# Kernel tuning notes

Measured on AMD Instinct MI355X. Metric: run time of the kernel, lower is better.

The kernel has to match this reference:

```python
import jax, jax.numpy as jnp
import numpy as np

N, E, F_IN, H, G, C, L = 100000, 1600000, 128, 128, 1000, 10, 3
EPS = 1e-5


def setup_inputs() -> dict:
    key = jax.random.key(0)
    ks = jax.random.split(key, 10)
    x = jax.random.normal(ks[0], (N, F_IN), dtype=jnp.float32)
    edge_index = jax.random.randint(ks[1], (2, E), 0, N, dtype=jnp.int64)
    batch = jnp.sort(jax.random.randint(ks[2], (N,), 0, G, dtype=jnp.int64))
    s = 1.0 / np.sqrt(H)
    conv_w = jax.random.normal(ks[3], (L, F_IN, H), dtype=jnp.float32) * s
    conv_b = jnp.zeros((L, H), dtype=jnp.float32)
    bn_gamma = jnp.ones((L, H), dtype=jnp.float32)
    bn_beta = jnp.zeros((L, H), dtype=jnp.float32)
    w1 = jax.random.normal(ks[4], (H, H // 2), dtype=jnp.float32) * s
    b1 = jnp.zeros((H // 2,), dtype=jnp.float32)
    w2 = jax.random.normal(ks[5], (H // 2, C), dtype=jnp.float32) * (1.0 / np.sqrt(H // 2))
    b2 = jnp.zeros((C,), dtype=jnp.float32)
    return {"x": x, "conv_w": conv_w, "conv_b": conv_b, "bn_gamma": bn_gamma,
            "bn_beta": bn_beta, "w1": w1, "b1": b1, "w2": w2, "b2": b2,
            "edge_index": edge_index, "batch": batch}


def _gcn_conv(x, w, b, src, dst):
    # PyG GCNConv: h = x @ W; symmetric-normalized aggregation with self-loops.
    h = x @ w  # [N, H]
    deg = 1.0 + jax.ops.segment_sum(jnp.ones((E,), x.dtype), dst, num_segments=N)
    dinv = jax.lax.rsqrt(deg)  # [N]
    norm = dinv[src] * dinv[dst]  # [E]
    agg = jax.ops.segment_sum(h[src] * norm[:, None], dst, num_segments=N)
    agg = agg + h * (dinv * dinv)[:, None]  # self-loop contribution
    return agg + b


def _batchnorm(x, gamma, beta):
    mean = jnp.mean(x, axis=0)
    var = jnp.mean(jnp.square(x - mean), axis=0)  # biased, as in torch BN fwd
    return gamma * (x - mean) * jax.lax.rsqrt(var + EPS) + beta


def reference(x, conv_w, conv_b, bn_gamma, bn_beta, w1, b1, w2, b2, edge_index, batch):
    src, dst = edge_index[0], edge_index[1]
    h = x
    for i in range(L):
        h = _gcn_conv(h, conv_w[i], conv_b[i], src, dst)
        h = _batchnorm(h, bn_gamma[i], bn_beta[i])
        h = jax.nn.relu(h)  # dropout is identity in eval mode
    # global mean pool over graphs
    sums = jax.ops.segment_sum(h, batch, num_segments=G)
    cnts = jax.ops.segment_sum(jnp.ones((N,), h.dtype), batch, num_segments=G)
    pooled = sums / jnp.maximum(cnts, 1.0)[:, None]
    # classifier MLP
    z = jax.nn.relu(pooled @ w1 + b1)
    return z @ w2 + b2
```

## Files before the change

kernel.cpp:

```cpp
#include <hip/hip_runtime.h>
#include <hip/hip_bf16.h>

#define N_NODES 100000
#define N_EDGES 1600000
#define HDIM    128
#define NGRAPH  1000
#define NCLASS  10
#define BN_EPS  1e-5f

#define BSHIFT  7
#define BMASK   127
#define NBUCKET 782
#define TILE3   8192
#define NSB     196
#define GATHER_BLOCKS 1024

typedef short short8_t __attribute__((ext_vector_type(8)));
typedef float f32x4_t  __attribute__((ext_vector_type(4)));

__device__ __forceinline__ float bf2f(ushort u) {
    union { unsigned int i; float f; } v; v.i = ((unsigned int)u) << 16; return v.f;
}
__device__ __forceinline__ ushort f2bf(float f) {
    union { float f; unsigned int i; } v; v.f = f;
    unsigned int i = v.i;
    unsigned int r = i + 0x7fffu + ((i >> 16) & 1u);
    return (ushort)(r >> 16);
}
__device__ __forceinline__ unsigned int pack2(float a, float b) {
    return (unsigned int)f2bf(a) | ((unsigned int)f2bf(b) << 16);
}
__device__ __forceinline__ float lo16(unsigned int u) {
    union { unsigned int i; float f; } v; v.i = u << 16; return v.f;
}
__device__ __forceinline__ float hi16(unsigned int u) {
    union { unsigned int i; float f; } v; v.i = u & 0xffff0000u; return v.f;
}

__global__ __launch_bounds__(256)
void wprep_hist(const float* __restrict__ W, ushort* __restrict__ wtbT,
                const int* __restrict__ dst, int* __restrict__ blockhist) {
    __shared__ int h[NBUCKET];
    int t = threadIdx.x;
    if (blockIdx.x < 48) {
        int l = blockIdx.x >> 4, slice = blockIdx.x & 15;
        int idx = slice * 1024 + t * 4;
        int k = idx >> 7, n = idx & 127;
        float4 w4 = *(const float4*)&W[(size_t)l * 16384 + k * 128 + n];
        ushort* o = wtbT + (size_t)l * 16384;
        o[(n + 0) * 128 + k] = f2bf(w4.x);
        o[(n + 1) * 128 + k] = f2bf(w4.y);
        o[(n + 2) * 128 + k] = f2bf(w4.z);
        o[(n + 3) * 128 + k] = f2bf(w4.w);
        return;
    }
    int blk = blockIdx.x - 48;
    for (int i = t; i < NBUCKET; i += 256) h[i] = 0;
    __syncthreads();
    long tile0 = (long)blk * TILE3;
    #pragma unroll 4
    for (int i = 0; i < TILE3 / 256; i++) {
        long e = tile0 + t + i * 256;
        if (e < N_EDGES) atomicAdd(&h[dst[e] >> BSHIFT], 1);
    }
    __syncthreads();
    for (int b = t; b < NBUCKET; b += 256)
        blockhist[(size_t)b * NSB + blk] = h[b];
}

__global__ __launch_bounds__(64)
void col_scan(int* __restrict__ blockhist, int* __restrict__ coltotal) {
    int b = blockIdx.x;
    int lane = threadIdx.x;
    int base = b * NSB;
    int carry = 0;
    for (int r = 0; r < NSB; r += 64) {
        int i = r + lane;
        int v = (i < NSB) ? blockhist[base + i] : 0;
        int x = v;
        #pragma unroll
        for (int off = 1; off < 64; off <<= 1) {
            int y = __shfl_up(x, off, 64);
            if (lane >= off) x += y;
        }
        if (i < NSB) blockhist[base + i] = carry + x - v;
        carry += __shfl(x, 63, 64);
    }
    if (lane == 0) coltotal[b] = carry;
}

__global__ __launch_bounds__(1024)
void bucket_scan(const int* __restrict__ coltotal, int* __restrict__ bucket_base,
                 int* __restrict__ row_start) {
    __shared__ int wsum[16];
    int t = threadIdx.x, lane = t & 63, wid = t >> 6;
    int v = (t < NBUCKET) ? coltotal[t] : 0;
    int x = v;
    #pragma unroll
    for (int off = 1; off < 64; off <<= 1) {
        int y = __shfl_up(x, off, 64);
        if (lane >= off) x += y;
    }
    if (lane == 63) wsum[wid] = x;
    __syncthreads();
    if (t == 0) {
        int s = 0;
        #pragma unroll
        for (int w = 0; w < 16; w++) { int tmp = wsum[w]; wsum[w] = s; s += tmp; }
    }
    __syncthreads();
    int excl = wsum[wid] + (x - v);
    if (t < NBUCKET) bucket_base[t] = excl;
    if (t == 0) { bucket_base[NBUCKET] = N_EDGES; row_start[N_NODES] = N_EDGES; }
}

__global__ __launch_bounds__(256)
void scatter_pairs(const int* __restrict__ src, const int* __restrict__ dst,
                   const int* __restrict__ bucket_base, const int* __restrict__ blockhist,
                   unsigned int* __restrict__ pairs) {
    __shared__ int lbase[NBUCKET];
    __shared__ int lcur[NBUCKET];
    int t = threadIdx.x;
    int blk = blockIdx.x;
    for (int b = t; b < NBUCKET; b += 256) {
        lbase[b] = bucket_base[b] + blockhist[(size_t)b * NSB + blk];
        lcur[b] = 0;
    }
    __syncthreads();
    long tile0 = (long)blk * TILE3;
    #pragma unroll 4
    for (int i = 0; i < TILE3 / 256; i++) {
        long e = tile0 + t + i * 256;
        if (e < N_EDGES) {
            int d = dst[e];
            int bkt = d >> BSHIFT;
            int p = atomicAdd(&lcur[bkt], 1);
            pairs[lbase[bkt] + p] = (unsigned int)src[e] | ((unsigned int)(d & BMASK) << 24);
        }
    }
}

__global__ __launch_bounds__(256)
void build_csr(const unsigned int* __restrict__ pairs, const int* __restrict__ bucket_base,
               int* __restrict__ row_start, int* __restrict__ csr_src, float* __restrict__ dinv) {
    __shared__ int hist[128];
    __shared__ int cur[128];
    __shared__ int wsum[2];
    int b = blockIdx.x;
    int t = threadIdx.x;
    int beg = bucket_base[b], end = bucket_base[b + 1];
    if (t < 128) hist[t] = 0;
    __syncthreads();
    for (int e = beg + t; e < end; e += 256)
        atomicAdd(&hist[pairs[e] >> 24], 1);
    __syncthreads();
    int v = 0, x = 0;
    int lane = t & 63, wid = t >> 6;
    if (t < 128) {
        v = hist[t];
        x = v;
        #pragma unroll
        for (int off = 1; off < 64; off <<= 1) {
            int y = __shfl_up(x, off, 64);
            if (lane >= off) x += y;
        }
        if (lane == 63) wsum[wid] = x;
    }
    __syncthreads();
    if (t == 0) { int s = wsum[0]; wsum[0] = 0; wsum[1] = s; }
    __syncthreads();
    if (t < 128) {
        int excl = wsum[wid] + (x - v);
        cur[t] = excl;
        int node = b * 128 + t;
        if (node < N_NODES) {
            row_start[node] = beg + excl;
            dinv[node] = rsqrtf(1.0f + (float)v);
        }
    }
    __syncthreads();
    for (int e = beg + t; e < end; e += 256) {
        unsigned int pk = pairs[e];
        int ln = pk >> 24;
        int sp = atomicAdd(&cur[ln], 1);
        csr_src[beg + sp] = (int)(pk & 0xFFFFFFu);
    }
}

__global__ __launch_bounds__(256)
void gemm_mfma(const float* __restrict__ inf, const ushort* __restrict__ inb,
               const ushort* __restrict__ wtbT, const float* __restrict__ bnp,
               const float* __restrict__ dinv, ushort* __restrict__ out) {
    __shared__ ushort as_[64][136];
    __shared__ ushort wt[128][136];
    int t = threadIdx.x;
    int wave = t >> 6, lane = t & 63;
    int g = lane >> 4, c = lane & 15;
    int rowbase = blockIdx.x * 64;

    #pragma unroll
    for (int i = 0; i < 8; i++) {
        int cid = t + i * 256;
        int n = cid >> 4, ko = (cid & 15) * 8;
        uint4 v = *(const uint4*)&wtbT[n * 128 + ko];
        *(uint4*)&wt[n][ko] = v;
    }
    if (inf) {
        #pragma unroll
        for (int i = 0; i < 8; i++) {
            int cid = t + i * 256;
            int r = cid >> 5, co = (cid & 31) * 4;
            int row = rowbase + r;
            ushort4 pk = make_ushort4(0, 0, 0, 0);
            if (row < N_NODES) {
                float4 v = *(const float4*)&inf[(size_t)row * HDIM + co];
                pk.x = f2bf(v.x); pk.y = f2bf(v.y); pk.z = f2bf(v.z); pk.w = f2bf(v.w);
            }
            *(ushort4*)&as_[r][co] = pk;
        }
    } else {
        #pragma unroll
        for (int i = 0; i < 4; i++) {
            int cid = t + i * 256;
            int r = cid >> 4, co = (cid & 15) * 8;
            int row = rowbase + r;
            uint4 o = make_uint4(0, 0, 0, 0);
            if (row < N_NODES) {
                uint4 p = *(const uint4*)&inb[(size_t)row * HDIM + co];
                float4 scA = *(const float4*)&bnp[co];
                float4 scB = *(const float4*)&bnp[co + 4];
                float4 shA = *(const float4*)&bnp[128 + co];
                float4 shB = *(const float4*)&bnp[132 + co];
                float v0 = fmaxf(0.f, fmaf(lo16(p.x), scA.x, shA.x));
                float v1 = fmaxf(0.f, fmaf(hi16(p.x), scA.y, shA.y));
                float v2 = fmaxf(0.f, fmaf(lo16(p.y), scA.z, shA.z));
                float v3 = fmaxf(0.f, fmaf(hi16(p.y), scA.w, shA.w));
                float v4 = fmaxf(0.f, fmaf(lo16(p.z), scB.x, shB.x));
                float v5 = fmaxf(0.f, fmaf(hi16(p.z), scB.y, shB.y));
                float v6 = fmaxf(0.f, fmaf(lo16(p.w), scB.z, shB.z));
                float v7 = fmaxf(0.f, fmaf(hi16(p.w), scB.w, shB.w));
                o.x = pack2(v0, v1); o.y = pack2(v2, v3);
                o.z = pack2(v4, v5); o.w = pack2(v6, v7);
            }
            *(uint4*)&as_[r][co] = o;
        }
    }
    __syncthreads();

    int m0 = wave * 16;
    short8_t a[4];
    #pragma unroll
    for (int ch = 0; ch < 4; ch++)
        a[ch] = *(const short8_t*)&as_[m0 + c][ch * 32 + g * 8];
    f32x4_t acc[8] = {};
    #pragma unroll
    for (int ct = 0; ct < 8; ct++) {
        #pragma unroll
        for (int ch = 0; ch < 4; ch++) {
            short8_t b = *(const short8_t*)&wt[ct * 16 + c][ch * 32 + g * 8];
            acc[ct] = __builtin_amdgcn_mfma_f32_16x16x32_bf16(a[ch], b, acc[ct], 0, 0, 0);
        }
    }
    float dv[4];
    #pragma unroll
    for (int reg = 0; reg < 4; reg++) {
        int rr = rowbase + m0 + g * 4 + reg;
        dv[reg] = dinv[rr < N_NODES ? rr : 0];
    }
    __syncthreads();
    #pragma unroll
    for (int ct = 0; ct < 8; ct++)
        #pragma unroll
        for (int reg = 0; reg < 4; reg++)
            as_[m0 + g * 4 + reg][ct * 16 + c] = f2bf(acc[ct][reg] * dv[reg]);
    __syncthreads();
    #pragma unroll
    for (int i = 0; i < 8; i++) {
        int cid = t + i * 256;
        int r = cid >> 5, co = (cid & 31) * 4;
        int row = rowbase + r;
        if (row < N_NODES)
            *(ushort4*)&out[(size_t)row * HDIM + co] = *(const ushort4*)&as_[r][co];
    }
}

__global__ __launch_bounds__(256)
void gather_agg(const ushort* __restrict__ hw, const int* __restrict__ row_start,
                const int* __restrict__ csr_src, const float* __restrict__ dinv,
                const float* __restrict__ bias, ushort* __restrict__ aggout,
                float* __restrict__ Spart, float* __restrict__ Qpart) {
    __shared__ float s_sum[128];
    __shared__ float s_sq[128];
    int t = threadIdx.x;
    if (t < 128) { s_sum[t] = 0.f; s_sq[t] = 0.f; }
    __syncthreads();
    int lane = t & 63, wid = t >> 6;
    int g = lane >> 4, c = lane & 15;
    int fo = c * 8;
    float4 bA = *(const float4*)&bias[fo];
    float4 bB = *(const float4*)&bias[fo + 4];
    float ls[8] = {}, lq[8] = {};
    int gw = blockIdx.x * 4 + wid;
    int nw = gridDim.x * 4;
    for (int n = gw; n < N_NODES; n += nw) {
        int jb = row_start[n], je = row_start[n + 1];
        float acc[8] = {};
        int j = jb;
        for (; j + 16 <= je; j += 16) {
            int s0 = csr_src[j + 4 * g + 0];
            int s1 = csr_src[j + 4 * g + 1];
            int s2 = csr_src[j + 4 * g + 2];
            int s3 = csr_src[j + 4 * g + 3];
            uint4 p0 = *(const uint4*)&hw[(size_t)s0 * HDIM + fo];
            uint4 p1 = *(const uint4*)&hw[(size_t)s1 * HDIM + fo];
            uint4 p2 = *(const uint4*)&hw[(size_t)s2 * HDIM + fo];
            uint4 p3 = *(const uint4*)&hw[(size_t)s3 * HDIM + fo];
            acc[0] += (lo16(p0.x) + lo16(p1.x)) + (lo16(p2.x) + lo16(p3.x));
            acc[1] += (hi16(p0.x) + hi16(p1.x)) + (hi16(p2.x) + hi16(p3.x));
            acc[2] += (lo16(p0.y) + lo16(p1.y)) + (lo16(p2.y) + lo16(p3.y));
            acc[3] += (hi16(p0.y) + hi16(p1.y)) + (hi16(p2.y) + hi16(p3.y));
            acc[4] += (lo16(p0.z) + lo16(p1.z)) + (lo16(p2.z) + lo16(p3.z));
            acc[5] += (hi16(p0.z) + hi16(p1.z)) + (hi16(p2.z) + hi16(p3.z));
            acc[6] += (lo16(p0.w) + lo16(p1.w)) + (lo16(p2.w) + lo16(p3.w));
            acc[7] += (hi16(p0.w) + hi16(p1.w)) + (hi16(p2.w) + hi16(p3.w));
        }
        for (; j + 8 <= je; j += 8) {
            int sa = csr_src[j + 2 * g];
            int sb = csr_src[j + 2 * g + 1];
            uint4 p = *(const uint4*)&hw[(size_t)sa * HDIM + fo];
            uint4 q = *(const uint4*)&hw[(size_t)sb * HDIM + fo];
            acc[0] += lo16(p.x) + lo16(q.x);
            acc[1] += hi16(p.x) + hi16(q.x);
            acc[2] += lo16(p.y) + lo16(q.y);
            acc[3] += hi16(p.y) + hi16(q.y);
            acc[4] += lo16(p.z) + lo16(q.z);
            acc[5] += hi16(p.z) + hi16(q.z);
            acc[6] += lo16(p.w) + lo16(q.w);
            acc[7] += hi16(p.w) + hi16(q.w);
        }
        int e0 = j + g, e1 = j + 4 + g;
        if (e0 < je) {
            int s = csr_src[e0];
            uint4 p = *(const uint4*)&hw[(size_t)s * HDIM + fo];
            acc[0] += lo16(p.x); acc[1] += hi16(p.x);
            acc[2] += lo16(p.y); acc[3] += hi16(p.y);
            acc[4] += lo16(p.z); acc[5] += hi16(p.z);
            acc[6] += lo16(p.w); acc[7] += hi16(p.w);
        }
        if (e1 < je) {
            int s = csr_src[e1];
            uint4 p = *(const uint4*)&hw[(size_t)s * HDIM + fo];
            acc[0] += lo16(p.x); acc[1] += hi16(p.x);
            acc[2] += lo16(p.y); acc[3] += hi16(p.y);
            acc[4] += lo16(p.z); acc[5] += hi16(p.z);
            acc[6] += lo16(p.w); acc[7] += hi16(p.w);
        }
        #pragma unroll
        for (int i = 0; i < 8; i++) {
            acc[i] += __shfl_xor(acc[i], 16);
            acc[i] += __shfl_xor(acc[i], 32);
        }
        uint4 ps = *(const uint4*)&hw[(size_t)n * HDIM + fo];
        float dn = dinv[n];
        float r[8];
        r[0] = fmaf(acc[0] + lo16(ps.x), dn, bA.x);
        r[1] = fmaf(acc[1] + hi16(ps.x), dn, bA.y);
        r[2] = fmaf(acc[2] + lo16(ps.y), dn, bA.z);
        r[3] = fmaf(acc[3] + hi16(ps.y), dn, bA.w);
        r[4] = fmaf(acc[4] + lo16(ps.z), dn, bB.x);
        r[5] = fmaf(acc[5] + hi16(ps.z), dn, bB.y);
        r[6] = fmaf(acc[6] + lo16(ps.w), dn, bB.z);
        r[7] = fmaf(acc[7] + hi16(ps.w), dn, bB.w);
        if (g == 0) {
            uint4 o;
            o.x = pack2(r[0], r[1]); o.y = pack2(r[2], r[3]);
            o.z = pack2(r[4], r[5]); o.w = pack2(r[6], r[7]);
            *(uint4*)&aggout[(size_t)n * HDIM + fo] = o;
            #pragma unroll
            for (int i = 0; i < 8; i++) { ls[i] += r[i]; lq[i] += r[i] * r[i]; }
        }
    }
    if (g == 0) {
        #pragma unroll
        for (int i = 0; i < 8; i++) {
            atomicAdd(&s_sum[fo + i], ls[i]);
            atomicAdd(&s_sq[fo + i],  lq[i]);
        }
    }
    __syncthreads();
    if (t < 128) {
        Spart[(size_t)blockIdx.x * 128 + t] = s_sum[t];
        Qpart[(size_t)blockIdx.x * 128 + t] = s_sq[t];
    }
}

__global__ __launch_bounds__(256)
void bn_reduce_prep(const float* __restrict__ Spart, const float* __restrict__ Qpart,
                    const float* __restrict__ gamma, const float* __restrict__ beta,
                    float* __restrict__ bnp) {
    __shared__ float rs[32][8];
    __shared__ float rq[32][8];
    int t = threadIdx.x;
    int fi = t & 7, chunk = t >> 3;
    int f = blockIdx.x * 8 + fi;
    float s = 0.f, q = 0.f;
    for (int b = chunk; b < GATHER_BLOCKS; b += 32) {
        s += Spart[(size_t)b * 128 + f];
        q += Qpart[(size_t)b * 128 + f];
    }
    rs[chunk][fi] = s; rq[chunk][fi] = q;
    __syncthreads();
    if (t < 8) {
        float S = 0.f, Q = 0.f;
        #pragma unroll
        for (int cc = 0; cc < 32; cc++) { S += rs[cc][t]; Q += rq[cc][t]; }
        int ff = blockIdx.x * 8 + t;
        float mean = S * (1.0f / N_NODES);
        float var  = Q * (1.0f / N_NODES) - mean * mean;
        float inv  = rsqrtf(var + BN_EPS);
        float sc   = gamma[ff] * inv;
        bnp[ff]       = sc;
        bnp[128 + ff] = beta[ff] - mean * sc;
    }
}

__global__ __launch_bounds__(128)
void pool_mlp(const ushort* __restrict__ agg, const float* __restrict__ bnp,
              const int* __restrict__ batch, const float* __restrict__ w1,
              const float* __restrict__ b1, const float* __restrict__ w2,
              const float* __restrict__ b2, float* __restrict__ out) {
    __shared__ float p[128];
    __shared__ float z[64];
    int g = blockIdx.x;
    int k = threadIdx.x;
    int lo = 0, hi = N_NODES;
    while (lo < hi) { int mid = (lo + hi) >> 1; if (batch[mid] < g) lo = mid + 1; else hi = mid; }
    int start = lo;
    hi = N_NODES;
    while (lo < hi) { int mid = (lo + hi) >> 1; if (batch[mid] < g + 1) lo = mid + 1; else hi = mid; }
    int end = lo;
    float sc = bnp[k], sh = bnp[128 + k];
    float sum = 0.f;
    int n = start;
    for (; n + 4 <= end; n += 4) {
        float a0 = bf2f(agg[(size_t)(n + 0) * HDIM + k]);
        float a1 = bf2f(agg[(size_t)(n + 1) * HDIM + k]);
        float a2 = bf2f(agg[(size_t)(n + 2) * HDIM + k]);
        float a3 = bf2f(agg[(size_t)(n + 3) * HDIM + k]);
        sum += fmaxf(0.f, fmaf(a0, sc, sh));
        sum += fmaxf(0.f, fmaf(a1, sc, sh));
        sum += fmaxf(0.f, fmaf(a2, sc, sh));
        sum += fmaxf(0.f, fmaf(a3, sc, sh));
    }
    for (; n < end; n++)
        sum += fmaxf(0.f, fmaf(bf2f(agg[(size_t)n * HDIM + k]), sc, sh));
    float cnt = (float)(end - start);
    p[k] = sum / fmaxf(cnt, 1.0f);
    __syncthreads();
    if (k < 64) {
        float s = b1[k];
        #pragma unroll 8
        for (int kk = 0; kk < 128; kk++) s += p[kk] * w1[kk * 64 + k];
        z[k] = fmaxf(0.f, s);
    }
    __syncthreads();
    if (k < NCLASS) {
        float s = b2[k];
        #pragma unroll
        for (int j = 0; j < 64; j++) s += z[j] * w2[j * NCLASS + k];
        out[g * NCLASS + k] = s;
    }
}

extern "C" void kernel_launch(void* const* d_in, const int* in_sizes, int n_in,
                              void* d_out, int out_size, void* d_ws, size_t ws_size,
                              hipStream_t stream) {
    const float* x      = (const float*)d_in[0];
    const float* conv_w = (const float*)d_in[1];
    const float* conv_b = (const float*)d_in[2];
    const float* gamma  = (const float*)d_in[3];
    const float* beta   = (const float*)d_in[4];
    const float* w1     = (const float*)d_in[5];
    const float* b1     = (const float*)d_in[6];
    const float* w2     = (const float*)d_in[7];
    const float* b2     = (const float*)d_in[8];
    const int*   ei     = (const int*)d_in[9];
    const int*   batch  = (const int*)d_in[10];
    float* out = (float*)d_out;

    char* ws = (char*)d_ws;
    size_t off = 0;
    auto alloc = [&](size_t bytes) -> void* {
        off = (off + 255) & ~(size_t)255;
        void* p = ws + off;
        off += bytes;
        return p;
    };
    ushort* A         = (ushort*)alloc((size_t)N_NODES * HDIM * 2);
    ushort* aggB      = (ushort*)alloc((size_t)N_NODES * HDIM * 2);
    int*    csr_src   = (int*)   alloc((size_t)N_EDGES * 4);
    int*    row_start = (int*)   alloc((size_t)(N_NODES + 1) * 4);
    float*  dinv      = (float*) alloc((size_t)N_NODES * 4);
    int*    blockhist = (int*)   alloc((size_t)NBUCKET * NSB * 4);
    int*    coltotal  = (int*)   alloc((size_t)NBUCKET * 4);
    int*    bbase     = (int*)   alloc((size_t)(NBUCKET + 1) * 4);
    ushort* wtbT      = (ushort*)alloc((size_t)3 * 16384 * 2);
    float*  Spart     = (float*) alloc((size_t)GATHER_BLOCKS * 128 * 4);
    float*  Qpart     = (float*) alloc((size_t)GATHER_BLOCKS * 128 * 4);
    float*  bnp       = (float*) alloc(3 * 256 * 4);
    unsigned int* pairs = (unsigned int*)aggB;

    const int* srcv = ei;
    const int* dstv = ei + N_EDGES;

    wprep_hist   <<<48 + NSB, 256, 0, stream>>>(conv_w, wtbT, dstv, blockhist);
    col_scan     <<<NBUCKET, 64, 0, stream>>>(blockhist, coltotal);
    bucket_scan  <<<1, 1024, 0, stream>>>(coltotal, bbase, row_start);
    scatter_pairs<<<NSB, 256, 0, stream>>>(srcv, dstv, bbase, blockhist, pairs);
    build_csr    <<<NBUCKET, 256, 0, stream>>>(pairs, bbase, row_start, csr_src, dinv);

    for (int l = 0; l < 3; l++) {
        gemm_mfma<<<(N_NODES + 63) / 64, 256, 0, stream>>>(
            (l == 0) ? x : nullptr, (l == 0) ? nullptr : aggB,
            wtbT + (size_t)l * 16384,
            (l == 0) ? nullptr : (bnp + (l - 1) * 256), dinv, A);
        gather_agg<<<GATHER_BLOCKS, 256, 0, stream>>>(A, row_start, csr_src, dinv,
                                                      conv_b + l * HDIM, aggB, Spart, Qpart);
        bn_reduce_prep<<<16, 256, 0, stream>>>(Spart, Qpart, gamma + l * HDIM,
                                               beta + l * HDIM, bnp + l * 256);
    }
    pool_mlp<<<NGRAPH, 128, 0, stream>>>(aggB, bnp + 2 * 256, batch, w1, b1, w2, b2, out);
}
```

Baseline: 499.8 us.

## Split feature dimension into two 64-wide planes for cache-local gathers

Stores node features as two contiguous 64-column planes instead of 128-wide rows, and runs the neighbor gather once per plane. Each pass touches a smaller working set, so random row gathers should hit cache more often. In exchange, the CSR indices are read twice, loads narrow to 8 bytes per lane, and there are extra kernel launches per layer.

```diff
diff --git a/kernel.cpp b/kernel.cpp
--- a/kernel.cpp
+++ b/kernel.cpp
@@ -14,6 +14,7 @@
 #define TILE3   8192
 #define NSB     196
 #define GATHER_BLOCKS 1024
+#define N64     ((size_t)N_NODES * 64)
 
 typedef short short8_t __attribute__((ext_vector_type(8)));
 typedef float f32x4_t  __attribute__((ext_vector_type(4)));
@@ -226,7 +227,7 @@
             int row = rowbase + r;
             uint4 o = make_uint4(0, 0, 0, 0);
             if (row < N_NODES) {
-                uint4 p = *(const uint4*)&inb[(size_t)row * HDIM + co];
+                uint4 p = *(const uint4*)&inb[(size_t)(co >> 6) * N64 + (size_t)row * 64 + (co & 63)];
                 float4 scA = *(const float4*)&bnp[co];
                 float4 scB = *(const float4*)&bnp[co + 4];
                 float4 shA = *(const float4*)&bnp[128 + co];
@@ -280,117 +281,112 @@
         int r = cid >> 5, co = (cid & 31) * 4;
         int row = rowbase + r;
         if (row < N_NODES)
-            *(ushort4*)&out[(size_t)row * HDIM + co] = *(const ushort4*)&as_[r][co];
+            *(ushort4*)&out[(size_t)(co >> 6) * N64 + (size_t)row * 64 + (co & 63)] =
+                *(const ushort4*)&as_[r][co];
     }
 }
 
 __global__ __launch_bounds__(256)
-void gather_agg(const ushort* __restrict__ hw, const int* __restrict__ row_start,
-                const int* __restrict__ csr_src, const float* __restrict__ dinv,
-                const float* __restrict__ bias, ushort* __restrict__ aggout,
-                float* __restrict__ Spart, float* __restrict__ Qpart) {
-    __shared__ float s_sum[128];
-    __shared__ float s_sq[128];
+void gather_slice(const ushort* __restrict__ hw, const int* __restrict__ row_start,
+                  const int* __restrict__ csr_src, const float* __restrict__ dinv,
+                  const float* __restrict__ bias, ushort* __restrict__ aggout,
+                  float* __restrict__ Spart, float* __restrict__ Qpart, int soff) {
+    __shared__ float s_sum[64];
+    __shared__ float s_sq[64];
     int t = threadIdx.x;
-    if (t < 128) { s_sum[t] = 0.f; s_sq[t] = 0.f; }
+    if (t < 64) { s_sum[t] = 0.f; s_sq[t] = 0.f; }
     __syncthreads();
     int lane = t & 63, wid = t >> 6;
     int g = lane >> 4, c = lane & 15;
-    int fo = c * 8;
+    int fo = c * 4;
     float4 bA = *(const float4*)&bias[fo];
-    float4 bB = *(const float4*)&bias[fo + 4];
-    float ls[8] = {}, lq[8] = {};
+    float ls[4] = {}, lq[4] = {};
     int gw = blockIdx.x * 4 + wid;
     int nw = gridDim.x * 4;
     for (int n = gw; n < N_NODES; n += nw) {
         int jb = row_start[n], je = row_start[n + 1];
-        float acc[8] = {};
+        float acc[4] = {};
         int j = jb;
-        for (; j + 16 <= je; j += 16) {
-            int s0 = csr_src[j + 4 * g + 0];
-            int s1 = csr_src[j + 4 * g + 1];
-            int s2 = csr_src[j + 4 * g + 2];
-            int s3 = csr_src[j + 4 * g + 3];
-            uint4 p0 = *(const uint4*)&hw[(size_t)s0 * HDIM + fo];
-            uint4 p1 = *(const uint4*)&hw[(size_t)s1 * HDIM + fo];
-            uint4 p2 = *(const uint4*)&hw[(size_t)s2 * HDIM + fo];
-            uint4 p3 = *(const uint4*)&hw[(size_t)s3 * HDIM + fo];
-            acc[0] += (lo16(p0.x) + lo16(p1.x)) + (lo16(p2.x) + lo16(p3.x));
-            acc[1] += (hi16(p0.x) + hi16(p1.x)) + (hi16(p2.x) + hi16(p3.x));
-            acc[2] += (lo16(p0.y) + lo16(p1.y)) + (lo16(p2.y) + lo16(p3.y));
-            acc[3] += (hi16(p0.y) + hi16(p1.y)) + (hi16(p2.y) + hi16(p3.y));
-            acc[4] += (lo16(p0.z) + lo16(p1.z)) + (lo16(p2.z) + lo16(p3.z));
-            acc[5] += (hi16(p0.z) + hi16(p1.z)) + (hi16(p2.z) + hi16(p3.z));
-            acc[6] += (lo16(p0.w) + lo16(p1.w)) + (lo16(p2.w) + lo16(p3.w));
-            acc[7] += (hi16(p0.w) + hi16(p1.w)) + (hi16(p2.w) + hi16(p3.w));
+        for (; j + 32 <= je; j += 32) {
+            int s0 = csr_src[j + 8 * g + 0];
+            int s1 = csr_src[j + 8 * g + 1];
+            int s2 = csr_src[j + 8 * g + 2];
+            int s3 = csr_src[j + 8 * g + 3];
+            int s4 = csr_src[j + 8 * g + 4];
+            int s5 = csr_src[j + 8 * g + 5];
+            int s6 = csr_src[j + 8 * g + 6];
+            int s7 = csr_src[j + 8 * g + 7];
+            uint2 p0 = *(const uint2*)&hw[(size_t)s0 * 64 + fo];
+            uint2 p1 = *(const uint2*)&hw[(size_t)s1 * 64 + fo];
+            uint2 p2 = *(const uint2*)&hw[(size_t)s2 * 64 + fo];
+            uint2 p3 = *(const uint2*)&hw[(size_t)s3 * 64 + fo];
+            uint2 p4 = *(const uint2*)&hw[(size_t)s4 * 64 + fo];
+            uint2 p5 = *(const uint2*)&hw[(size_t)s5 * 64 + fo];
+            uint2 p6 = *(const uint2*)&hw[(size_t)s6 * 64 + fo];
+            uint2 p7 = *(const uint2*)&hw[(size_t)s7 * 64 + fo];
+            acc[0] += ((lo16(p0.x) + lo16(p1.x)) + (lo16(p2.x) + lo16(p3.x)))
+                    + ((lo16(p4.x) + lo16(p5.x)) + (lo16(p6.x) + lo16(p7.x)));
+            acc[1] += ((hi16(p0.x) + hi16(p1.x)) + (hi16(p2.x) + hi16(p3.x)))
+                    + ((hi16(p4.x) + hi16(p5.x)) + (hi16(p6.x) + hi16(p7.x)));
+            acc[2] += ((lo16(p0.y) + lo16(p1.y)) + (lo16(p2.y) + lo16(p3.y)))
+                    + ((lo16(p4.y) + lo16(p5.y)) + (lo16(p6.y) + lo16(p7.y)));
+            acc[3] += ((hi16(p0.y) + hi16(p1.y)) + (hi16(p2.y) + hi16(p3.y)))
+                    + ((hi16(p4.y) + hi16(p5.y)) + (hi16(p6.y) + hi16(p7.y)));
         }
         for (; j + 8 <= je; j += 8) {
             int sa = csr_src[j + 2 * g];
             int sb = csr_src[j + 2 * g + 1];
-            uint4 p = *(const uint4*)&hw[(size_t)sa * HDIM + fo];
-            uint4 q = *(const uint4*)&hw[(size_t)sb * HDIM + fo];
+            uint2 p = *(const uint2*)&hw[(size_t)sa * 64 + fo];
+            uint2 q = *(const uint2*)&hw[(size_t)sb * 64 + fo];
             acc[0] += lo16(p.x) + lo16(q.x);
             acc[1] += hi16(p.x) + hi16(q.x);
             acc[2] += lo16(p.y) + lo16(q.y);
             acc[3] += hi16(p.y) + hi16(q.y);
-            acc[4] += lo16(p.z) + lo16(q.z);
-            acc[5] += hi16(p.z) + hi16(q.z);
-            acc[6] += lo16(p.w) + lo16(q.w);
-            acc[7] += hi16(p.w) + hi16(q.w);
         }
         int e0 = j + g, e1 = j + 4 + g;
         if (e0 < je) {
             int s = csr_src[e0];
-            uint4 p = *(const uint4*)&hw[(size_t)s * HDIM + fo];
+            uint2 p = *(const uint2*)&hw[(size_t)s * 64 + fo];
             acc[0] += lo16(p.x); acc[1] += hi16(p.x);
             acc[2] += lo16(p.y); acc[3] += hi16(p.y);
-            acc[4] += lo16(p.z); acc[5] += hi16(p.z);
-            acc[6] += lo16(p.w); acc[7] += hi16(p.w);
         }
         if (e1 < je) {
             int s = csr_src[e1];
-            uint4 p = *(const uint4*)&hw[(size_t)s * HDIM + fo];
+            uint2 p = *(const uint2*)&hw[(size_t)s * 64 + fo];
             acc[0] += lo16(p.x); acc[1] += hi16(p.x);
             acc[2] += lo16(p.y); acc[3] += hi16(p.y);
-            acc[4] += lo16(p.z); acc[5] += hi16(p.z);
-            acc[6] += lo16(p.w); acc[7] += hi16(p.w);
-        }
-        #pragma unroll
-        for (int i = 0; i < 8; i++) {
+        }
+        #pragma unroll
+        for (int i = 0; i < 4; i++) {
             acc[i] += __shfl_xor(acc[i], 16);
             acc[i] += __shfl_xor(acc[i], 32);
         }
-        uint4 ps = *(const uint4*)&hw[(size_t)n * HDIM + fo];
+        uint2 ps = *(const uint2*)&hw[(size_t)n * 64 + fo];
         float dn = dinv[n];
-        float r[8];
+        float r[4];
         r[0] = fmaf(acc[0] + lo16(ps.x), dn, bA.x);
         r[1] = fmaf(acc[1] + hi16(ps.x), dn, bA.y);
         r[2] = fmaf(acc[2] + lo16(ps.y), dn, bA.z);
         r[3] = fmaf(acc[3] + hi16(ps.y), dn, bA.w);
-        r[4] = fmaf(acc[4] + lo16(ps.z), dn, bB.x);
-        r[5] = fmaf(acc[5] + hi16(ps.z), dn, bB.y);
-        r[6] = fmaf(acc[6] + lo16(ps.w), dn, bB.z);
-        r[7] = fmaf(acc[7] + hi16(ps.w), dn, bB.w);
         if (g == 0) {
-            uint4 o;
-            o.x = pack2(r[0], r[1]); o.y = pack2(r[2], r[3]);
-            o.z = pack2(r[4], r[5]); o.w = pack2(r[6], r[7]);
-            *(uint4*)&aggout[(size_t)n * HDIM + fo] = o;
+            ushort4 o;
+            o.x = f2bf(r[0]); o.y = f2bf(r[1]); o.z = f2bf(r[2]); o.w = f2bf(r[3]);
+            *(ushort4*)&aggout[(size_t)n * 64 + fo] = o;
             #pragma unroll
-            for (int i = 0; i < 8; i++) { ls[i] += r[i]; lq[i] += r[i] * r[i]; }
+            for (int i = 0; i < 4; i++) { ls[i] += r[i]; lq[i] += r[i] * r[i]; }
         }
     }
     if (g == 0) {
         #pragma unroll
-        for (int i = 0; i < 8; i++) {
+        for (int i = 0; i < 4; i++) {
             atomicAdd(&s_sum[fo + i], ls[i]);
             atomicAdd(&s_sq[fo + i],  lq[i]);
         }
     }
     __syncthreads();
-    if (t < 128) {
-        Spart[(size_t)blockIdx.x * 128 + t] = s_sum[t];
-        Qpart[(size_t)blockIdx.x * 128 + t] = s_sq[t];
+    if (t < 64) {
+        Spart[(size_t)blockIdx.x * 128 + soff + t] = s_sum[t];
+        Qpart[(size_t)blockIdx.x * 128 + soff + t] = s_sq[t];
     }
 }
 
@@ -439,21 +435,22 @@
     hi = N_NODES;
     while (lo < hi) { int mid = (lo + hi) >> 1; if (batch[mid] < g + 1) lo = mid + 1; else hi = mid; }
     int end = lo;
+    const ushort* base = agg + (size_t)(k >> 6) * N64 + (k & 63);
     float sc = bnp[k], sh = bnp[128 + k];
     float sum = 0.f;
     int n = start;
     for (; n + 4 <= end; n += 4) {
-        float a0 = bf2f(agg[(size_t)(n + 0) * HDIM + k]);
-        float a1 = bf2f(agg[(size_t)(n + 1) * HDIM + k]);
-        float a2 = bf2f(agg[(size_t)(n + 2) * HDIM + k]);
-        float a3 = bf2f(agg[(size_t)(n + 3) * HDIM + k]);
+        float a0 = bf2f(base[(size_t)(n + 0) * 64]);
+        float a1 = bf2f(base[(size_t)(n + 1) * 64]);
+        float a2 = bf2f(base[(size_t)(n + 2) * 64]);
+        float a3 = bf2f(base[(size_t)(n + 3) * 64]);
         sum += fmaxf(0.f, fmaf(a0, sc, sh));
         sum += fmaxf(0.f, fmaf(a1, sc, sh));
         sum += fmaxf(0.f, fmaf(a2, sc, sh));
         sum += fmaxf(0.f, fmaf(a3, sc, sh));
     }
     for (; n < end; n++)
-        sum += fmaxf(0.f, fmaf(bf2f(agg[(size_t)n * HDIM + k]), sc, sh));
+        sum += fmaxf(0.f, fmaf(bf2f(base[(size_t)n * 64]), sc, sh));
     float cnt = (float)(end - start);
     p[k] = sum / fmaxf(cnt, 1.0f);
     __syncthreads();
@@ -524,8 +521,12 @@
             (l == 0) ? x : nullptr, (l == 0) ? nullptr : aggB,
             wtbT + (size_t)l * 16384,
             (l == 0) ? nullptr : (bnp + (l - 1) * 256), dinv, A);
-        gather_agg<<<GATHER_BLOCKS, 256, 0, stream>>>(A, row_start, csr_src, dinv,
-                                                      conv_b + l * HDIM, aggB, Spart, Qpart);
+        for (int s = 0; s < 2; s++) {
+            gather_slice<<<GATHER_BLOCKS, 256, 0, stream>>>(
+                A + (size_t)s * N64, row_start, csr_src, dinv,
+                conv_b + l * HDIM + s * 64, aggB + (size_t)s * N64,
+                Spart, Qpart, s * 64);
+        }
         bn_reduce_prep<<<16, 256, 0, stream>>>(Spart, Qpart, gamma + l * HDIM,
                                                beta + l * HDIM, bnp + l * 256);
     }
```

Result: slower. 696.9 us (+39.4%).
